# Kernel tuning notes

Hardware: AMD Instinct MI355X
Metric: run time of the kernel (lower is better)

The kernel has to match this reference:

```python
import jax, jax.numpy as jnp
import numpy as np
from jax import lax

C, K, G = 256, 3, 8
CG = C // G          # group channels
P = K * K            # sampling points per group
STRIDE, PAD, DIL = 1, 1, 1
OFFSET_SCALE = 1.0
EPS = 1e-5


def setup_inputs() -> dict:
    key = jax.random.key(0)
    ks = jax.random.split(key, 8)
    N, H, W = 4, 64, 64
    return {
        "x": jax.random.normal(ks[0], (N, C, H, W), jnp.float32),
        "dw_w": jax.random.normal(ks[1], (C, 1, K, K), jnp.float32) * 0.1,
        "dw_b": jax.random.normal(ks[2], (C,), jnp.float32) * 0.01,
        "gn_g": jnp.ones((C,), jnp.float32),
        "gn_b": jnp.zeros((C,), jnp.float32),
        "off_w": jax.random.normal(ks[3], (C, G * P * 2), jnp.float32) * 0.01,
        "off_b": jax.random.normal(ks[4], (G * P * 2,), jnp.float32) * 0.1,
        "mask_w": jax.random.normal(ks[5], (C, G * P), jnp.float32) * 0.02,
        "mask_b": jax.random.normal(ks[6], (G * P,), jnp.float32) * 0.02,
    }


def _dcnv3_core(x_nhwc, offset, mask):
    # x_nhwc (N,H,W,C); offset (N,Ho,Wo,G*P*2); mask (N,Ho,Wo,G*P) already softmaxed
    inp = jnp.pad(x_nhwc, ((0, 0), (PAD, PAD), (PAD, PAD), (0, 0)))
    N, Hp, Wp, _ = inp.shape
    Ho = (Hp - (DIL * (K - 1) + 1)) // STRIDE + 1
    Wo = (Wp - (DIL * (K - 1) + 1)) // STRIDE + 1
    base = (DIL * (K - 1)) // 2 + 0.5
    ref_y = (base + jnp.arange(Ho, dtype=jnp.float32) * STRIDE) / Hp  # (Ho,)
    ref_x = (base + jnp.arange(Wo, dtype=jnp.float32) * STRIDE) / Wp  # (Wo,)
    # dilation grid; flatten order p = iw*K + ih (matches torch meshgrid(x,y) ij)
    kvals = jnp.arange(K, dtype=jnp.float32) * DIL - (DIL * (K - 1)) // 2
    gx = jnp.repeat(kvals, K) / Wp  # (P,)
    gy = jnp.tile(kvals, K) / Hp    # (P,)
    off = offset.reshape(N, Ho, Wo, G, P, 2)
    # normalized sampling locations in [0,1] (then grid_sample convention 2*loc-1)
    loc_x = ref_x[None, None, :, None, None] + gx * OFFSET_SCALE + off[..., 0] * OFFSET_SCALE / Wp
    loc_y = ref_y[None, :, None, None, None] + gy * OFFSET_SCALE + off[..., 1] * OFFSET_SCALE / Hp
    # pixel coords, align_corners=False: px = loc*size - 0.5
    px = loc_x * Wp - 0.5
    py = loc_y * Hp - 0.5
    x0 = jnp.floor(px)
    y0 = jnp.floor(py)
    wx = px - x0
    wy = py - y0
    x0i = x0.astype(jnp.int32)
    y0i = y0.astype(jnp.int32)

    inp_flat = inp.reshape(N, Hp * Wp, G, CG)
    n_idx = jnp.arange(N)[:, None, None, None, None]
    g_idx = jnp.arange(G)[None, None, None, :, None]

    def gather(yi, xi):
        # zeros padding: clamp index, zero out-of-bounds corners
        valid = (yi >= 0) & (yi < Hp) & (xi >= 0) & (xi < Wp)
        idx = jnp.clip(yi, 0, Hp - 1) * Wp + jnp.clip(xi, 0, Wp - 1)
        v = inp_flat[n_idx, idx, g_idx]  # (N,Ho,Wo,G,P,CG)
        return v * valid[..., None]

    m = mask.reshape(N, Ho, Wo, G, P)
    out = jnp.zeros((N, Ho, Wo, G, CG), jnp.float32)
    for dy, dx, w in ((0, 0, (1 - wy) * (1 - wx)), (0, 1, (1 - wy) * wx),
                      (1, 0, wy * (1 - wx)), (1, 1, wy * wx)):
        v = gather(y0i + dy, x0i + dx)
        out = out + jnp.einsum('nhwgp,nhwgpc->nhwgc', m * w, v)
    return out.reshape(N, Ho, Wo, G * CG)


def reference(x, dw_w, dw_b, gn_g, gn_b, off_w, off_b, mask_w, mask_b):
    N, _, H, W = x.shape
    # depthwise 3x3 conv (groups=channels)
    x1 = lax.conv_general_dilated(
        x, dw_w, (1, 1), [((K - 1) // 2, (K - 1) // 2)] * 2,
        dimension_numbers=('NCHW', 'OIHW', 'NCHW'), feature_group_count=C)
    x1 = x1 + dw_b[None, :, None, None]
    # GroupNorm with num_groups=1: normalize over (C,H,W) per sample
    mu = jnp.mean(x1, axis=(1, 2, 3), keepdims=True)
    var = jnp.mean((x1 - mu) ** 2, axis=(1, 2, 3), keepdims=True)
    x1 = (x1 - mu) * lax.rsqrt(var + EPS)
    x1 = x1 * gn_g[None, :, None, None] + gn_b[None, :, None, None]
    x1 = jax.nn.gelu(x1, approximate=False)
    x1 = jnp.transpose(x1, (0, 2, 3, 1))  # NHWC
    offset = x1 @ off_w + off_b                                  # (N,H,W,G*P*2)
    mask = jax.nn.softmax((x1 @ mask_w + mask_b).reshape(N, H, W, G, P), axis=-1)
    mask = mask.reshape(N, H, W, G * P)
    out = _dcnv3_core(jnp.transpose(x, (0, 2, 3, 1)), offset, mask)
    return jnp.transpose(out, (0, 3, 1, 2))  # back to NCHW
```

## Files before the change

### kernel.cpp

```cpp
#include <hip/hip_runtime.h>
#include <math.h>

#define NB   4
#define CH   256
#define HW   4096
#define NCOL 216
#define MTOT 16384
#define CHW  1048576
#define EPSV 1e-5f

#define OFF_NHWC 0
#define NHWCSZ   (NB*HW*CH/2)
#define OFF_OM   (OFF_NHWC + NHWCSZ)
#define OMSZ     (MTOT*NCOL/2)
#define OFF_AB   (OFF_OM + OMSZ)
#define ABSZ     (MTOT*CH/2)
#define OFF_WB   (OFF_AB + ABSZ)
#define WBSZ     (CH*CH/2)
#define OFF_BI   (OFF_WB + WBSZ)
#define OFF_PT   (OFF_BI + 256)

typedef short bf16x8 __attribute__((ext_vector_type(8)));
typedef float f32x4  __attribute__((ext_vector_type(4)));

__device__ __forceinline__ unsigned short f2bf(float f) {
    unsigned int u = __builtin_bit_cast(unsigned int, f);
    u += 0x7fffu + ((u >> 16) & 1u);
    return (unsigned short)(u >> 16);
}

__device__ __forceinline__ float bf2f(unsigned short s) {
    return __builtin_bit_cast(float, (unsigned int)s << 16);
}

__global__ __launch_bounds__(256) void conv_prep_kernel(
    const float* __restrict__ x, const float* __restrict__ dw_w,
    const float* __restrict__ dw_b,
    const float* __restrict__ off_w, const float* __restrict__ off_b,
    const float* __restrict__ mask_w, const float* __restrict__ mask_b,
    unsigned short* __restrict__ A, unsigned short* __restrict__ inp_nhwc,
    unsigned short* __restrict__ Wc_bt, float* __restrict__ bias,
    float* __restrict__ partials) {
    __shared__ float xs[32 * 108];
    __shared__ unsigned short tb[32 * 36];
    __shared__ float rs1[256], rs2[256];
    int b = blockIdx.x;
    int tid = threadIdx.x;
    if (b < 256) {
        int k = b, n = tid;
        float v = 0.f;
        if (n < 144)      v = off_w[k * 144 + n];
        else if (n < 216) v = mask_w[k * 72 + (n - 144)];
        Wc_bt[(size_t)n * 256 + k] = f2bf(v);
        if (b == 0) {
            float bb = 0.f;
            if (n < 144)      bb = off_b[n];
            else if (n < 216) bb = mask_b[n - 144];
            bias[n] = bb;
        }
    }
    int ct  = b & 7;
    int hwt = (b >> 3) & 127;
    int n   = b >> 10;
    int c0 = ct * 32;
    int hw0 = hwt * 32;
    int h  = hw0 >> 6;
    int w0 = hw0 & 63;
    const float* xb = x + ((size_t)n * CH + c0) * HW;
    for (int it = 0; it < 13; ++it) {
        int q = it * 256 + tid;
        if (q < 3264) {
            int cl = q / 102;
            int rr = q - cl * 102;
            int r  = rr / 34;
            int i  = rr - r * 34;
            int gh = h - 1 + r;
            int gw = w0 - 1 + i;
            float v = 0.f;
            if (gh >= 0 && gh < 64 && gw >= 0 && gw < 64)
                v = xb[(size_t)cl * HW + gh * 64 + gw];
            xs[cl * 108 + r * 36 + i] = v;
        }
    }
    __syncthreads();
    int wl = tid & 31;
    int cbase = (tid >> 5) * 4;
    float s1 = 0.f, s2 = 0.f;
    ushort4 o;
    unsigned short ov[4];
#pragma unroll
    for (int j = 0; j < 4; ++j) {
        int c = c0 + cbase + j;
        float acc = dw_b[c];
        const float* wk = dw_w + c * 9;
#pragma unroll
        for (int r = 0; r < 3; ++r)
#pragma unroll
            for (int kx = 0; kx < 3; ++kx)
                acc = fmaf(xs[(cbase + j) * 108 + r * 36 + wl + kx], wk[r * 3 + kx], acc);
        s1 += acc; s2 += acc * acc;
        ov[j] = f2bf(acc);
    }
    o.x = ov[0]; o.y = ov[1]; o.z = ov[2]; o.w = ov[3];
    *(ushort4*)&tb[wl * 36 + cbase] = o;
    rs1[tid] = s1; rs2[tid] = s2;
    {
        int r2 = tid >> 3, cg = tid & 7;
        ushort4 rv;
        rv.x = f2bf(xs[(cg * 4 + 0) * 108 + 36 + r2 + 1]);
        rv.y = f2bf(xs[(cg * 4 + 1) * 108 + 36 + r2 + 1]);
        rv.z = f2bf(xs[(cg * 4 + 2) * 108 + 36 + r2 + 1]);
        rv.w = f2bf(xs[(cg * 4 + 3) * 108 + 36 + r2 + 1]);
        *(ushort4*)&inp_nhwc[((size_t)(n * HW + hw0 + r2)) * 256 + c0 + cg * 4] = rv;
    }
    __syncthreads();
    for (int s = 128; s > 0; s >>= 1) {
        if (tid < s) { rs1[tid] += rs1[tid + s]; rs2[tid] += rs2[tid + s]; }
        __syncthreads();
    }
    if (tid == 0) {
        partials[2 * b]     = rs1[0];
        partials[2 * b + 1] = rs2[0];
    }
    int r2 = tid >> 3, cg = tid & 7;
    ushort4 w4 = *(const ushort4*)&tb[r2 * 36 + cg * 4];
    *(ushort4*)&A[((size_t)(n * HW + hw0 + r2)) * 256 + c0 + cg * 4] = w4;
}

__global__ __launch_bounds__(256) void stats_kernel(
    const float* __restrict__ partials, float* __restrict__ stats) {
    __shared__ float r1[256], r2[256];
    int n = blockIdx.x, tid = threadIdx.x;
    float s1 = 0.f, s2 = 0.f;
    for (int i = tid; i < 1024; i += 256) {
        s1 += partials[2 * (n * 1024 + i)];
        s2 += partials[2 * (n * 1024 + i) + 1];
    }
    r1[tid] = s1; r2[tid] = s2;
    __syncthreads();
    for (int s = 128; s > 0; s >>= 1) {
        if (tid < s) { r1[tid] += r1[tid + s]; r2[tid] += r2[tid + s]; }
        __syncthreads();
    }
    if (tid == 0) {
        float mean = r1[0] * (1.f / (float)CHW);
        float var  = r2[0] * (1.f / (float)CHW) - mean * mean;
        stats[2 * n]     = mean;
        stats[2 * n + 1] = rsqrtf(var + EPSV);
    }
}

#define LDK 72
__global__ __launch_bounds__(512) void gemm_fused_kernel(
    const unsigned short* __restrict__ A, const unsigned short* __restrict__ Bt,
    const float* __restrict__ bias, const float* __restrict__ stats,
    const float* __restrict__ gn_g, const float* __restrict__ gn_b,
    unsigned short* __restrict__ offmask) {
    __shared__ unsigned short As[64 * LDK];
    __shared__ unsigned short Bs[256 * LDK];
    int m0 = blockIdx.x * 64;
    int n = m0 >> 12;
    int tid = threadIdx.x, lane = tid & 63, wid = tid >> 6;
    float mean = stats[2 * n];
    float rsig = stats[2 * n + 1];
    f32x4 acc[4][2] = {};
    for (int k0 = 0; k0 < 256; k0 += 64) {
        {
            int row = tid >> 3, kk0 = (tid & 7) * 8;
            union { uint4 u; unsigned short s[8]; } in, ou;
            in.u = *(const uint4*)&A[((size_t)(m0 + row)) * 256 + k0 + kk0];
#pragma unroll
            for (int j = 0; j < 8; ++j) {
                int ch = k0 + kk0 + j;
                float v = bf2f(in.s[j]);
                v = (v - mean) * rsig * gn_g[ch] + gn_b[ch];
                v = 0.5f * v * (1.0f + erff(v * 0.70710678118654752f));
                ou.s[j] = f2bf(v);
            }
            *(uint4*)&As[row * LDK + kk0] = ou.u;
        }
#pragma unroll
        for (int i = 0; i < 4; ++i) {
            int q = i * 512 + tid;
            int mm = q >> 3, kk = (q & 7) * 8;
            *(uint4*)&Bs[mm * LDK + kk] = *(const uint4*)&Bt[(size_t)mm * 256 + k0 + kk];
        }
        __syncthreads();
#pragma unroll
        for (int kh = 0; kh < 2; ++kh) {
            bf16x8 af[4], bfr[2];
#pragma unroll
            for (int mi = 0; mi < 4; ++mi)
                af[mi] = *(const bf16x8*)&As[(mi * 16 + (lane & 15)) * LDK + kh * 32 + (lane >> 4) * 8];
#pragma unroll
            for (int nj = 0; nj < 2; ++nj)
                bfr[nj] = *(const bf16x8*)&Bs[(wid * 32 + nj * 16 + (lane & 15)) * LDK + kh * 32 + (lane >> 4) * 8];
#pragma unroll
            for (int mi = 0; mi < 4; ++mi)
#pragma unroll
                for (int nj = 0; nj < 2; ++nj)
                    acc[mi][nj] = __builtin_amdgcn_mfma_f32_16x16x32_bf16(
                        af[mi], bfr[nj], acc[mi][nj], 0, 0, 0);
        }
        __syncthreads();
    }
#pragma unroll
    for (int nj = 0; nj < 2; ++nj) {
        int col = wid * 32 + nj * 16 + (lane & 15);
        if (col < NCOL) {
            float bcol = bias[col];
#pragma unroll
            for (int mi = 0; mi < 4; ++mi)
#pragma unroll
                for (int r = 0; r < 4; ++r) {
                    int row = m0 + mi * 16 + (lane >> 4) * 4 + r;
                    offmask[(size_t)row * NCOL + col] = f2bf(acc[mi][nj][r] + bcol);
                }
        }
    }
}

__global__ __launch_bounds__(256) void dcn_out_kernel(
    const unsigned short* __restrict__ inp_nhwc, const unsigned short* __restrict__ offmask,
    float* __restrict__ out) {
    __shared__ float lom[8 * 216];
    __shared__ float ot[8 * 260];
    int bid = blockIdx.x;
    int swz = (bid & 7) * 256 + (bid >> 3);
    int tid = threadIdx.x;
    int pix0 = swz * 8;
    int n = pix0 >> 12;
    int hwb = pix0 & 4095;
    {
        const unsigned int* om2 = (const unsigned int*)(offmask + (size_t)pix0 * NCOL);
        for (int i = tid; i < 8 * NCOL / 2; i += 256) {
            unsigned int v = om2[i];
            lom[2 * i]     = bf2f((unsigned short)(v & 0xffffu));
            lom[2 * i + 1] = bf2f((unsigned short)(v >> 16));
        }
    }
    __syncthreads();
    int pixloc = tid >> 5;
    int l  = tid & 31;
    int g  = l >> 2;
    int ch0 = l * 8;
    const unsigned short* base = inp_nhwc + (size_t)n * HW * 256;
    int hw = hwb + pixloc;
    int h = hw >> 6, w = hw & 63;
    const float* lm = &lom[pixloc * NCOL];
    float lg[9];
    float mx = -1e30f;
#pragma unroll
    for (int p = 0; p < 9; ++p) { lg[p] = lm[144 + g * 9 + p]; mx = fmaxf(mx, lg[p]); }
    float sum = 0.f;
#pragma unroll
    for (int p = 0; p < 9; ++p) { lg[p] = __expf(lg[p] - mx); sum += lg[p]; }
    float rs = 1.0f / sum;
    float acc[8] = {};
#pragma unroll
    for (int p = 0; p < 9; ++p) {
        float ox = lm[g * 18 + p * 2];
        float oy = lm[g * 18 + p * 2 + 1];
        float px = (float)(w + (p / 3)) + ox;
        float py = (float)(h + (p % 3)) + oy;
        float xf = floorf(px), yf = floorf(py);
        float wx = px - xf, wy = py - yf;
        int x0 = (int)xf, y0 = (int)yf;
        float m = lg[p] * rs;
        float w00 = m * (1.f - wy) * (1.f - wx);
        float w01 = m * (1.f - wy) * wx;
        float w10 = m * wy * (1.f - wx);
        float w11 = m * wy * wx;
#pragma unroll
        for (int corner = 0; corner < 4; ++corner) {
            int yi = y0 + (corner >> 1);
            int xi = x0 + (corner & 1);
            float cw = (corner == 0) ? w00 : (corner == 1) ? w01 : (corner == 2) ? w10 : w11;
            bool valid = (yi >= 1) & (yi <= 64) & (xi >= 1) & (xi <= 64);
            int yc = min(max(yi, 1), 64) - 1;
            int xc = min(max(xi, 1), 64) - 1;
            bf16x8 v = *(const bf16x8*)&base[((size_t)yc * 64 + xc) * 256 + ch0];
            float f = valid ? cw : 0.f;
#pragma unroll
            for (int j = 0; j < 8; ++j)
                acc[j] = fmaf(f, bf2f((unsigned short)v[j]), acc[j]);
        }
    }
    *(float4*)&ot[pixloc * 260 + ch0]     = make_float4(acc[0], acc[1], acc[2], acc[3]);
    *(float4*)&ot[pixloc * 260 + ch0 + 4] = make_float4(acc[4], acc[5], acc[6], acc[7]);
    __syncthreads();
    int px = tid & 7, crow = tid >> 3;
#pragma unroll
    for (int cc = 0; cc < 8; ++cc) {
        int c = cc * 32 + crow;
        out[((size_t)(n * CH + c)) * HW + hwb + px] = ot[px * 260 + c];
    }
}

extern "C" void kernel_launch(void* const* d_in, const int* in_sizes, int n_in,
                              void* d_out, int out_size, void* d_ws, size_t ws_size,
                              hipStream_t stream) {
    const float* x      = (const float*)d_in[0];
    const float* dw_w   = (const float*)d_in[1];
    const float* dw_b   = (const float*)d_in[2];
    const float* gn_g   = (const float*)d_in[3];
    const float* gn_b   = (const float*)d_in[4];
    const float* off_w  = (const float*)d_in[5];
    const float* off_b  = (const float*)d_in[6];
    const float* mask_w = (const float*)d_in[7];
    const float* mask_b = (const float*)d_in[8];
    float* out = (float*)d_out;

    float* ws = (float*)d_ws;
    unsigned short* inp_nhwc = (unsigned short*)(ws + OFF_NHWC);
    unsigned short* offmask  = (unsigned short*)(ws + OFF_OM);
    unsigned short* Abf   = (unsigned short*)(ws + OFF_AB);
    unsigned short* Wc_bt = (unsigned short*)(ws + OFF_WB);
    float* bias     = ws + OFF_BI;
    float* partials = ws + OFF_PT;
    float* stats    = ws + OFF_BI + 240;

    conv_prep_kernel<<<4096, 256, 0, stream>>>(x, dw_w, dw_b, off_w, off_b,
                                               mask_w, mask_b, Abf, inp_nhwc,
                                               Wc_bt, bias, partials);
    stats_kernel<<<4, 256, 0, stream>>>(partials, stats);
    gemm_fused_kernel<<<256, 512, 0, stream>>>(Abf, Wc_bt, bias, stats,
                                               gn_g, gn_b, offmask);
    dcn_out_kernel<<<2048, 256, 0, stream>>>(inp_nhwc, offmask, out);
}
```

Before: 146.1 us.

## Fuse stats reduction, offset/mask GEMM, and deformable sampling into one kernel

Removes the separate stats kernel and the dcn_out kernel. Each GEMM block now reduces the GroupNorm partials itself, keeps the 64x216 offset/mask tile in shared memory as fp32, and then runs the bilinear sampling for its 64 pixels in four rounds of 16. This cuts two launches and the global round-trip of the bf16 offmask buffer, and keeps offsets at fp32. The cost is only 256 blocks of 512 threads with much larger shared memory (about 80KB), so occupancy and parallelism in the gather-heavy sampling phase drop. Every block also repeats the partials reduction.

```diff
diff --git a/kernel.cpp b/kernel.cpp
--- a/kernel.cpp
+++ b/kernel.cpp
@@ -127,42 +127,41 @@
     *(ushort4*)&A[((size_t)(n * HW + hw0 + r2)) * 256 + c0 + cg * 4] = w4;
 }
 
-__global__ __launch_bounds__(256) void stats_kernel(
-    const float* __restrict__ partials, float* __restrict__ stats) {
-    __shared__ float r1[256], r2[256];
-    int n = blockIdx.x, tid = threadIdx.x;
-    float s1 = 0.f, s2 = 0.f;
-    for (int i = tid; i < 1024; i += 256) {
-        s1 += partials[2 * (n * 1024 + i)];
-        s2 += partials[2 * (n * 1024 + i) + 1];
-    }
-    r1[tid] = s1; r2[tid] = s2;
-    __syncthreads();
-    for (int s = 128; s > 0; s >>= 1) {
-        if (tid < s) { r1[tid] += r1[tid + s]; r2[tid] += r2[tid + s]; }
-        __syncthreads();
-    }
-    if (tid == 0) {
-        float mean = r1[0] * (1.f / (float)CHW);
-        float var  = r2[0] * (1.f / (float)CHW) - mean * mean;
-        stats[2 * n]     = mean;
-        stats[2 * n + 1] = rsqrtf(var + EPSV);
-    }
-}
-
 #define LDK 72
-__global__ __launch_bounds__(512) void gemm_fused_kernel(
+__global__ __launch_bounds__(512) void fused_gemm_dcn_kernel(
     const unsigned short* __restrict__ A, const unsigned short* __restrict__ Bt,
-    const float* __restrict__ bias, const float* __restrict__ stats,
+    const float* __restrict__ bias, const float* __restrict__ partials,
     const float* __restrict__ gn_g, const float* __restrict__ gn_b,
-    unsigned short* __restrict__ offmask) {
+    const unsigned short* __restrict__ inp_nhwc, float* __restrict__ out) {
     __shared__ unsigned short As[64 * LDK];
     __shared__ unsigned short Bs[256 * LDK];
-    int m0 = blockIdx.x * 64;
+    __shared__ float lom[64 * 216];
+    __shared__ float ot[16 * 260];
+    __shared__ float red1[512], red2[512];
+
+    int bid = blockIdx.x;
+    int tile = (bid & 7) * 32 + (bid >> 3);
+    int m0 = tile * 64;
     int n = m0 >> 12;
+    int hwb = m0 & 4095;
     int tid = threadIdx.x, lane = tid & 63, wid = tid >> 6;
-    float mean = stats[2 * n];
-    float rsig = stats[2 * n + 1];
+
+    {
+        const float2* p2 = (const float2*)partials;
+        float2 a = p2[n * 1024 + tid];
+        float2 c = p2[n * 1024 + tid + 512];
+        red1[tid] = a.x + c.x;
+        red2[tid] = a.y + c.y;
+    }
+    __syncthreads();
+    for (int s = 256; s > 0; s >>= 1) {
+        if (tid < s) { red1[tid] += red1[tid + s]; red2[tid] += red2[tid + s]; }
+        __syncthreads();
+    }
+    float mean = red1[0] * (1.f / (float)CHW);
+    float var  = red2[0] * (1.f / (float)CHW) - mean * mean;
+    float rsig = rsqrtf(var + EPSV);
+
     f32x4 acc[4][2] = {};
     for (int k0 = 0; k0 < 256; k0 += 64) {
         {
@@ -213,87 +212,72 @@
             for (int mi = 0; mi < 4; ++mi)
 #pragma unroll
                 for (int r = 0; r < 4; ++r) {
-                    int row = m0 + mi * 16 + (lane >> 4) * 4 + r;
-                    offmask[(size_t)row * NCOL + col] = f2bf(acc[mi][nj][r] + bcol);
+                    int row = mi * 16 + (lane >> 4) * 4 + r;
+                    lom[row * NCOL + col] = acc[mi][nj][r] + bcol;
                 }
         }
     }
-}
-
-__global__ __launch_bounds__(256) void dcn_out_kernel(
-    const unsigned short* __restrict__ inp_nhwc, const unsigned short* __restrict__ offmask,
-    float* __restrict__ out) {
-    __shared__ float lom[8 * 216];
-    __shared__ float ot[8 * 260];
-    int bid = blockIdx.x;
-    int swz = (bid & 7) * 256 + (bid >> 3);
-    int tid = threadIdx.x;
-    int pix0 = swz * 8;
-    int n = pix0 >> 12;
-    int hwb = pix0 & 4095;
-    {
-        const unsigned int* om2 = (const unsigned int*)(offmask + (size_t)pix0 * NCOL);
-        for (int i = tid; i < 8 * NCOL / 2; i += 256) {
-            unsigned int v = om2[i];
-            lom[2 * i]     = bf2f((unsigned short)(v & 0xffffu));
-            lom[2 * i + 1] = bf2f((unsigned short)(v >> 16));
-        }
-    }
     __syncthreads();
-    int pixloc = tid >> 5;
+
+    const unsigned short* base = inp_nhwc + (size_t)n * HW * 256;
+    int h = hwb >> 6;
+    int half = tid >> 5;
     int l  = tid & 31;
     int g  = l >> 2;
     int ch0 = l * 8;
-    const unsigned short* base = inp_nhwc + (size_t)n * HW * 256;
-    int hw = hwb + pixloc;
-    int h = hw >> 6, w = hw & 63;
-    const float* lm = &lom[pixloc * NCOL];
-    float lg[9];
-    float mx = -1e30f;
-#pragma unroll
-    for (int p = 0; p < 9; ++p) { lg[p] = lm[144 + g * 9 + p]; mx = fmaxf(mx, lg[p]); }
-    float sum = 0.f;
-#pragma unroll
-    for (int p = 0; p < 9; ++p) { lg[p] = __expf(lg[p] - mx); sum += lg[p]; }
-    float rs = 1.0f / sum;
-    float acc[8] = {};
-#pragma unroll
-    for (int p = 0; p < 9; ++p) {
-        float ox = lm[g * 18 + p * 2];
-        float oy = lm[g * 18 + p * 2 + 1];
-        float px = (float)(w + (p / 3)) + ox;
-        float py = (float)(h + (p % 3)) + oy;
-        float xf = floorf(px), yf = floorf(py);
-        float wx = px - xf, wy = py - yf;
-        int x0 = (int)xf, y0 = (int)yf;
-        float m = lg[p] * rs;
-        float w00 = m * (1.f - wy) * (1.f - wx);
-        float w01 = m * (1.f - wy) * wx;
-        float w10 = m * wy * (1.f - wx);
-        float w11 = m * wy * wx;
-#pragma unroll
-        for (int corner = 0; corner < 4; ++corner) {
-            int yi = y0 + (corner >> 1);
-            int xi = x0 + (corner & 1);
-            float cw = (corner == 0) ? w00 : (corner == 1) ? w01 : (corner == 2) ? w10 : w11;
-            bool valid = (yi >= 1) & (yi <= 64) & (xi >= 1) & (xi <= 64);
-            int yc = min(max(yi, 1), 64) - 1;
-            int xc = min(max(xi, 1), 64) - 1;
-            bf16x8 v = *(const bf16x8*)&base[((size_t)yc * 64 + xc) * 256 + ch0];
-            float f = valid ? cw : 0.f;
-#pragma unroll
-            for (int j = 0; j < 8; ++j)
-                acc[j] = fmaf(f, bf2f((unsigned short)v[j]), acc[j]);
-        }
-    }
-    *(float4*)&ot[pixloc * 260 + ch0]     = make_float4(acc[0], acc[1], acc[2], acc[3]);
-    *(float4*)&ot[pixloc * 260 + ch0 + 4] = make_float4(acc[4], acc[5], acc[6], acc[7]);
-    __syncthreads();
-    int px = tid & 7, crow = tid >> 3;
-#pragma unroll
-    for (int cc = 0; cc < 8; ++cc) {
-        int c = cc * 32 + crow;
-        out[((size_t)(n * CH + c)) * HW + hwb + px] = ot[px * 260 + c];
+#pragma unroll
+    for (int round = 0; round < 4; ++round) {
+        int pixloc = round * 16 + half;
+        int w = pixloc;
+        const float* lm = &lom[pixloc * NCOL];
+        float lg[9];
+        float mx = -1e30f;
+#pragma unroll
+        for (int p = 0; p < 9; ++p) { lg[p] = lm[144 + g * 9 + p]; mx = fmaxf(mx, lg[p]); }
+        float sum = 0.f;
+#pragma unroll
+        for (int p = 0; p < 9; ++p) { lg[p] = __expf(lg[p] - mx); sum += lg[p]; }
+        float rs = 1.0f / sum;
+        float acc2[8] = {};
+#pragma unroll
+        for (int p = 0; p < 9; ++p) {
+            float ox = lm[g * 18 + p * 2];
+            float oy = lm[g * 18 + p * 2 + 1];
+            float px = (float)(w + (p / 3)) + ox;
+            float py = (float)(h + (p % 3)) + oy;
+            float xf = floorf(px), yf = floorf(py);
+            float wx = px - xf, wy = py - yf;
+            int x0 = (int)xf, y0 = (int)yf;
+            float m = lg[p] * rs;
+            float w00 = m * (1.f - wy) * (1.f - wx);
+            float w01 = m * (1.f - wy) * wx;
+            float w10 = m * wy * (1.f - wx);
+            float w11 = m * wy * wx;
+#pragma unroll
+            for (int corner = 0; corner < 4; ++corner) {
+                int yi = y0 + (corner >> 1);
+                int xi = x0 + (corner & 1);
+                float cw = (corner == 0) ? w00 : (corner == 1) ? w01 : (corner == 2) ? w10 : w11;
+                bool valid = (yi >= 1) & (yi <= 64) & (xi >= 1) & (xi <= 64);
+                int yc = min(max(yi, 1), 64) - 1;
+                int xc = min(max(xi, 1), 64) - 1;
+                bf16x8 v = *(const bf16x8*)&base[((size_t)yc * 64 + xc) * 256 + ch0];
+                float f = valid ? cw : 0.f;
+#pragma unroll
+                for (int j = 0; j < 8; ++j)
+                    acc2[j] = fmaf(f, bf2f((unsigned short)v[j]), acc2[j]);
+            }
+        }
+        *(float4*)&ot[half * 260 + ch0]     = make_float4(acc2[0], acc2[1], acc2[2], acc2[3]);
+        *(float4*)&ot[half * 260 + ch0 + 4] = make_float4(acc2[4], acc2[5], acc2[6], acc2[7]);
+        __syncthreads();
+        int px = tid & 15, crow = tid >> 4;
+#pragma unroll
+        for (int cc = 0; cc < 8; ++cc) {
+            int c = cc * 32 + crow;
+            out[((size_t)(n * CH + c)) * HW + hwb + round * 16 + px] = ot[px * 260 + c];
+        }
+        __syncthreads();
     }
 }
 
@@ -313,18 +297,14 @@
 
     float* ws = (float*)d_ws;
     unsigned short* inp_nhwc = (unsigned short*)(ws + OFF_NHWC);
-    unsigned short* offmask  = (unsigned short*)(ws + OFF_OM);
     unsigned short* Abf   = (unsigned short*)(ws + OFF_AB);
     unsigned short* Wc_bt = (unsigned short*)(ws + OFF_WB);
     float* bias     = ws + OFF_BI;
     float* partials = ws + OFF_PT;
-    float* stats    = ws + OFF_BI + 240;
 
     conv_prep_kernel<<<4096, 256, 0, stream>>>(x, dw_w, dw_b, off_w, off_b,
                                                mask_w, mask_b, Abf, inp_nhwc,
                                                Wc_bt, bias, partials);
-    stats_kernel<<<4, 256, 0, stream>>>(partials, stats);
-    gemm_fused_kernel<<<256, 512, 0, stream>>>(Abf, Wc_bt, bias, stats,
-                                               gn_g, gn_b, offmask);
-    dcn_out_kernel<<<2048, 256, 0, stream>>>(inp_nhwc, offmask, out);
-}
+    fused_gemm_dcn_kernel<<<256, 512, 0, stream>>>(Abf, Wc_bt, bias, partials,
+                                                   gn_g, gn_b, inp_nhwc, out);
+}
```

New measurement: 140.7 us. -3.7%, faster.
